# Kernel optimization log

Hardware: AMD Instinct MI355X
Metric: run time of the kernel (lower is better)

Reference implementation:

```python
import jax, jax.numpy as jnp
import numpy as np

D = 1024
N_HEADS = 16
HEAD = D // N_HEADS


def apply_rope(x):
    # x: [b, h, s, hd]
    b, h, s, hd = x.shape
    half = hd // 2
    pos = jnp.arange(1, s + 1, dtype=jnp.float32)  # positions start at 1 (as in source)
    thetas = 10000.0 ** (-2.0 * jnp.arange(half, dtype=jnp.float32) / hd)
    angles = pos[:, None] * thetas[None, :]  # [s, half]
    cos, sin = jnp.cos(angles), jnp.sin(angles)
    x_even, x_odd = x[..., 0::2], x[..., 1::2]
    out_even = x_even * cos - x_odd * sin
    out_odd = x_odd * cos + x_even * sin
    # interleave back: stack on new last axis then reshape
    return jnp.stack([out_even, out_odd], axis=-1).reshape(b, h, s, hd)


def setup_inputs() -> dict:
    key = jax.random.key(0)
    k1, k2, k3 = jax.random.split(key, 3)
    b, s = 4, 2048
    x = jax.random.normal(k1, (b, s, D), dtype=jnp.float32)
    # torch Linear(d, 3d, bias=False): y = x @ W.T; store as [d, 3d] so y = x @ W_qkv
    W_qkv = jax.random.normal(k2, (D, 3 * D), dtype=jnp.float32) * (1.0 / np.sqrt(D))
    W_out = jax.random.normal(k3, (D, D), dtype=jnp.float32) * (1.0 / np.sqrt(D))
    return {"x": x, "W_qkv": W_qkv, "W_out": W_out}


def reference(x, W_qkv, W_out):
    b, s, _ = x.shape
    qkv = x @ W_qkv  # [b, s, 3d]
    q, k, v = jnp.split(qkv, 3, axis=-1)

    def split_heads(t):
        return t.reshape(b, s, N_HEADS, HEAD).transpose(0, 2, 1, 3)  # [b,h,s,hd]

    q, k, v = split_heads(q), split_heads(k), split_heads(v)
    q, k = apply_rope(q), apply_rope(k)
    scale = 1.0 / np.sqrt(HEAD)
    scores = jnp.einsum("bhqd,bhkd->bhqk", q, k) * scale
    attn = jax.nn.softmax(scores, axis=-1)
    out = jnp.einsum("bhqk,bhkd->bhqd", attn, v)  # [b,h,s,hd]
    out = out.transpose(0, 2, 1, 3).reshape(b, s, D)
    return out @ W_out
```

## Files before the change

### kernel.cpp

```cpp
#include <hip/hip_runtime.h>
#include <hip/hip_bf16.h>
#include <math.h>

#define BB 4
#define SS 2048
#define DD 1024
#define NH 16
#define HD 64

typedef __attribute__((ext_vector_type(8))) short bf16x8;
typedef __attribute__((ext_vector_type(4))) float f32x4;

#define MFMA16(a, b, c) __builtin_amdgcn_mfma_f32_16x16x32_bf16(a, b, c, 0, 0, 0)

#if __has_builtin(__builtin_amdgcn_exp2f)
#define EXP2(x) __builtin_amdgcn_exp2f(x)
#else
#define EXP2(x) exp2f(x)
#endif

__device__ __forceinline__ ushort f2bf(float f) {
    unsigned int u = __builtin_bit_cast(unsigned int, f);
    u += 0x7FFF + ((u >> 16) & 1);
    return (ushort)(u >> 16);
}
__device__ __forceinline__ float bf2f(ushort u) {
    return __builtin_bit_cast(float, (unsigned)u << 16);
}
__device__ __forceinline__ unsigned pk2bf(float a, float b) {
    __hip_bfloat162 h = __float22bfloat162_rn(make_float2(a, b));
    unsigned r;
    __builtin_memcpy(&r, &h, 4);
    return r;
}

__device__ __forceinline__ void gload16(const void* g, void* l) {
    __builtin_amdgcn_global_load_lds(
        (const __attribute__((address_space(1))) void*)g,
        (__attribute__((address_space(3))) void*)l, 16, 0, 0);
}

__global__ __launch_bounds__(256)
void prep_kernel(const float* __restrict__ X, ushort* __restrict__ Xb,
                 const float* __restrict__ Wqkv, ushort* __restrict__ Wqt,
                 const float* __restrict__ Wout, ushort* __restrict__ Wot,
                 float2* __restrict__ tab)
{
    const int blk = blockIdx.x;
    const int t = threadIdx.x;
    if (blk < 4096) {
        const size_t i = ((size_t)blk * 256 + t) * 8;
        const float4 v0 = *(const float4*)&X[i];
        const float4 v1 = *(const float4*)&X[i + 4];
        uint4 o;
        o.x = pk2bf(v0.x, v0.y);
        o.y = pk2bf(v0.z, v0.w);
        o.z = pk2bf(v1.x, v1.y);
        o.w = pk2bf(v1.z, v1.w);
        *(uint4*)&Xb[i] = o;
    } else if (blk < 5120) {
        __shared__ ushort T[64][72];
        const bool isQ = blk < 4864;
        const int b2 = isQ ? blk - 4096 : blk - 4864;
        const int ncols = isQ ? 3072 : 1024;
        const float* W = isQ ? Wqkv : Wout;
        ushort* Wt = isQ ? Wqt : Wot;
        const int ki = b2 / (ncols / 64), ni = b2 % (ncols / 64);
        const int k0 = ki * 64, n0 = ni * 64;
        #pragma unroll
        for (int e = 0; e < 4; ++e) {
            const int idx = t + e * 256;
            const int kr = idx >> 4, c4 = (idx & 15) * 4;
            const float4 v = *(const float4*)&W[(size_t)(k0 + kr) * ncols + n0 + c4];
            T[c4 + 0][kr] = f2bf(v.x); T[c4 + 1][kr] = f2bf(v.y);
            T[c4 + 2][kr] = f2bf(v.z); T[c4 + 3][kr] = f2bf(v.w);
        }
        __syncthreads();
        #pragma unroll
        for (int e = 0; e < 2; ++e) {
            const int idx = t + e * 256;
            const int nr = idx >> 3, kc = (idx & 7) * 8;
            uint4 o;
            o.x = (unsigned)T[nr][kc + 0] | ((unsigned)T[nr][kc + 1] << 16);
            o.y = (unsigned)T[nr][kc + 2] | ((unsigned)T[nr][kc + 3] << 16);
            o.z = (unsigned)T[nr][kc + 4] | ((unsigned)T[nr][kc + 5] << 16);
            o.w = (unsigned)T[nr][kc + 6] | ((unsigned)T[nr][kc + 7] << 16);
            *(uint4*)&Wt[(size_t)(n0 + nr) * 1024 + k0 + kc] = o;
        }
    } else {
        const int id = (blk - 5120) * 256 + t;
        const int s = id >> 5, i = id & 31;
        const float theta = expf(-0.28782313662425572f * (float)i);
        const float ang = (float)(s + 1) * theta;
        float sn, cs;
        sincosf(ang, &sn, &cs);
        tab[id] = make_float2(cs, sn);
    }
}

__global__ __launch_bounds__(256)
void rope_cast_kernel(ushort* __restrict__ Qi, ushort* __restrict__ Ki,
                      const float2* __restrict__ tab)
{
    const int HALFT = BB * NH * SS * 8;
    const int tid = blockIdx.x * 256 + threadIdx.x;
    const bool isK = tid >= HALFT;
    const int rr = isK ? tid - HALFT : tid;
    ushort* buf = isK ? Ki : Qi;
    const float sc = isK ? 1.0f : 0.180336880111112f;

    const int row = rr >> 3;
    const int e8  = rr & 7;
    const int s   = row & (SS - 1);
    const size_t base = (size_t)row * HD + e8 * 8;
    const uint4 iv = *(const uint4*)&buf[base];
    const unsigned ua[4] = {iv.x, iv.y, iv.z, iv.w};

    uint4 o;
    unsigned ow[4];
    #pragma unroll
    for (int j = 0; j < 4; ++j) {
        const float xe = __builtin_bit_cast(float, ua[j] << 16);
        const float xo = __builtin_bit_cast(float, ua[j] & 0xffff0000u);
        const float2 cs = tab[s * 32 + e8 * 4 + j];
        const float oe = (xe * cs.x - xo * cs.y) * sc;
        const float oo = (xo * cs.x + xe * cs.y) * sc;
        ow[j] = pk2bf(oe, oo);
    }
    o.x = ow[0]; o.y = ow[1]; o.z = ow[2]; o.w = ow[3];
    *(uint4*)&buf[base] = o;
}

template<int K, int NI>
__global__ __launch_bounds__(256)
void gemm_bt_kernel(const ushort* __restrict__ Ag, const ushort* __restrict__ Btg,
                    ushort* __restrict__ D0, ushort* __restrict__ D1,
                    ushort* __restrict__ D2)
{
    __shared__ ushort Ab[2][128 * 32];
    __shared__ ushort Bb[2][128 * 32];
    const int t = threadIdx.x, lane = t & 63, w = t >> 6;
    const int lo = lane & 15, g = lane >> 4;
    const int wr = w >> 1, wc = w & 1;

    const int nwg = gridDim.x;
    const int bid = blockIdx.x;
    const int wg = (bid & 7) * (nwg >> 3) + (bid >> 3);
    const int m0 = (wg / NI) * 128, n0 = (wg % NI) * 128;

    const int srow  = lane >> 2;
    const int sslot = (lane & 3) ^ ((srow >> 1) & 3);

    f32x4 acc[4][4];
    #pragma unroll
    for (int m = 0; m < 4; ++m)
        #pragma unroll
        for (int n = 0; n < 4; ++n)
            acc[m][n] = (f32x4){0.f, 0.f, 0.f, 0.f};

#define STAGE(kt, bb)                                                              \
    {                                                                              \
        const int kk = (kt) * 32;                                                  \
        _Pragma("unroll")                                                          \
        for (int e = 0; e < 2; ++e) {                                              \
            const int r0 = w * 32 + e * 16;                                        \
            gload16(Ag  + (size_t)(m0 + r0 + srow) * K + kk + sslot * 8,           \
                    &Ab[bb][r0 * 32]);                                             \
            gload16(Btg + (size_t)(n0 + r0 + srow) * K + kk + sslot * 8,           \
                    &Bb[bb][r0 * 32]);                                             \
        }                                                                          \
    }

    const int NKS = K / 32;
    STAGE(0, 0)
    for (int kt = 0; kt < NKS; ++kt) {
        const int cur = kt & 1;
        if (kt + 1 < NKS) {
            STAGE(kt + 1, cur ^ 1)
            asm volatile("s_waitcnt vmcnt(4)" ::: "memory");
        } else {
            asm volatile("s_waitcnt vmcnt(0)" ::: "memory");
        }
        __builtin_amdgcn_sched_barrier(0);
        __builtin_amdgcn_s_barrier();

        const int xsl = ((g ^ ((lo >> 1) & 3)) << 3);
        bf16x8 af[4], bfr[4];
        #pragma unroll
        for (int m = 0; m < 4; ++m)
            af[m] = *(const bf16x8*)&Ab[cur][(wr * 64 + m * 16 + lo) * 32 + xsl];
        #pragma unroll
        for (int n = 0; n < 4; ++n)
            bfr[n] = *(const bf16x8*)&Bb[cur][(wc * 64 + n * 16 + lo) * 32 + xsl];
        #pragma unroll
        for (int m = 0; m < 4; ++m)
            #pragma unroll
            for (int n = 0; n < 4; ++n)
                acc[m][n] = MFMA16(af[m], bfr[n], acc[m][n]);

        asm volatile("s_waitcnt lgkmcnt(0)" ::: "memory");
        __builtin_amdgcn_sched_barrier(0);
        __builtin_amdgcn_s_barrier();
    }
#undef STAGE

    const int tensor = n0 >> 10;
    const int cb = n0 & 1023;
    if (tensor == 2) {
        #pragma unroll
        for (int m = 0; m < 4; ++m) {
            const int row0 = m0 + wr * 64 + m * 16 + g * 4;
            const int b = row0 >> 11, sbase = row0 & (SS - 1);
            #pragma unroll
            for (int n = 0; n < 4; ++n) {
                const int c = cb + wc * 64 + n * 16 + lo;
                const int h = c >> 6, d = c & 63;
                uint2 wv = make_uint2(pk2bf(acc[m][n][0], acc[m][n][1]),
                                      pk2bf(acc[m][n][2], acc[m][n][3]));
                *(uint2*)&D2[(((size_t)b * NH + h) * HD + d) * SS + sbase] = wv;
            }
        }
    } else {
        ushort* dst = (tensor == 0) ? D0 : D1;
        const bool evlane = (lo & 1) == 0;
        #pragma unroll
        for (int m = 0; m < 4; ++m)
            #pragma unroll
            for (int n = 0; n < 4; ++n) {
                const int c = cb + wc * 64 + n * 16 + lo;
                const int h = c >> 6, d = c & 63;
                #pragma unroll
                for (int r = 0; r < 4; ++r) {
                    const int row = m0 + wr * 64 + m * 16 + g * 4 + r;
                    const float x  = acc[m][n][r];
                    const float xp = __shfl_xor(x, 1);
                    if (evlane) {
                        const int b = row >> 11, s = row & (SS - 1);
                        *(unsigned*)&dst[(((size_t)b * NH + h) * SS + s) * HD + d] =
                            pk2bf(x, xp);
                    }
                }
            }
    }
}

template<int K>
__global__ __launch_bounds__(256)
void gemm_bt64_kernel(const ushort* __restrict__ Ag, const ushort* __restrict__ Btg,
                      float* __restrict__ Df)
{
    __shared__ ushort Ab[2][128 * 32];
    __shared__ ushort Bb[2][64 * 32];
    const int t = threadIdx.x, lane = t & 63, w = t >> 6;
    const int lo = lane & 15, g = lane >> 4;
    const int NI = 16;

    const int nwg = gridDim.x;
    const int bid = blockIdx.x;
    const int wg = (bid & 7) * (nwg >> 3) + (bid >> 3);
    const int m0 = (wg / NI) * 128, n0 = (wg % NI) * 64;

    const int srow  = lane >> 2;
    const int sslot = (lane & 3) ^ ((srow >> 1) & 3);

    f32x4 acc[2][4];
    #pragma unroll
    for (int m = 0; m < 2; ++m)
        #pragma unroll
        for (int n = 0; n < 4; ++n)
            acc[m][n] = (f32x4){0.f, 0.f, 0.f, 0.f};

#define STAGE(kt, bb)                                                              \
    {                                                                              \
        const int kk = (kt) * 32;                                                  \
        _Pragma("unroll")                                                          \
        for (int e = 0; e < 2; ++e) {                                              \
            const int r0 = w * 32 + e * 16;                                        \
            gload16(Ag + (size_t)(m0 + r0 + srow) * K + kk + sslot * 8,            \
                    &Ab[bb][r0 * 32]);                                             \
        }                                                                          \
        gload16(Btg + (size_t)(n0 + w * 16 + srow) * K + kk + sslot * 8,           \
                &Bb[bb][(w * 16) * 32]);                                           \
    }

    const int NKS = K / 32;
    STAGE(0, 0)
    for (int kt = 0; kt < NKS; ++kt) {
        const int cur = kt & 1;
        if (kt + 1 < NKS) {
            STAGE(kt + 1, cur ^ 1)
            asm volatile("s_waitcnt vmcnt(3)" ::: "memory");
        } else {
            asm volatile("s_waitcnt vmcnt(0)" ::: "memory");
        }
        __builtin_amdgcn_sched_barrier(0);
        __builtin_amdgcn_s_barrier();

        const int xsl = ((g ^ ((lo >> 1) & 3)) << 3);
        bf16x8 af[2], bfr[4];
        #pragma unroll
        for (int m = 0; m < 2; ++m)
            af[m] = *(const bf16x8*)&Ab[cur][(w * 32 + m * 16 + lo) * 32 + xsl];
        #pragma unroll
        for (int n = 0; n < 4; ++n)
            bfr[n] = *(const bf16x8*)&Bb[cur][(n * 16 + lo) * 32 + xsl];
        #pragma unroll
        for (int m = 0; m < 2; ++m)
            #pragma unroll
            for (int n = 0; n < 4; ++n)
                acc[m][n] = MFMA16(af[m], bfr[n], acc[m][n]);

        asm volatile("s_waitcnt lgkmcnt(0)" ::: "memory");
        __builtin_amdgcn_sched_barrier(0);
        __builtin_amdgcn_s_barrier();
    }
#undef STAGE

    const bool evlane = (lo & 1) == 0;
    #pragma unroll
    for (int m = 0; m < 2; ++m)
        #pragma unroll
        for (int n = 0; n < 4; ++n) {
            const int col = n0 + n * 16 + lo;
            #pragma unroll
            for (int r = 0; r < 4; ++r) {
                const int row = m0 + w * 32 + m * 16 + g * 4 + r;
                const float x  = acc[m][n][r];
                const float xp = __shfl_xor(x, 1);
                if (evlane)
                    *(float2*)&Df[(size_t)row * 1024 + col] = make_float2(x, xp);
            }
        }
}

__global__ __launch_bounds__(256, 4)
void attn_mfma_kernel(const ushort* __restrict__ Qbf, const ushort* __restrict__ Kbf,
                      const ushort* __restrict__ Vt, ushort* __restrict__ Obt)
{
    __shared__ ushort Ks[2][4096];
    __shared__ ushort Vs[2][4096];
    __shared__ ushort Ps[4][1024];

    const int t    = threadIdx.x;
    const int lane = t & 63;
    const int w    = t >> 6;
    const int g    = lane >> 4;
    const int lo   = lane & 15;
    const int lo7  = lo & 7;
    const int wmask = lo & 6;

    const int i  = blockIdx.x;
    const int r_ = i & 63;
    const int bh = (r_ & 7) * 8 + (r_ >> 3);
    const int qt = i >> 6;

    const size_t kbase  = (size_t)bh * SS * HD;
    const size_t vtbase = (size_t)bh * HD * SS;
    const int s0 = qt * 128;

    bf16x8 qa[2][2];
    #pragma unroll
    for (int qh = 0; qh < 2; ++qh)
        #pragma unroll
        for (int df = 0; df < 2; ++df)
            qa[qh][df] = *(const bf16x8*)
                &Qbf[kbase + (size_t)(s0 + w * 32 + qh * 16 + lo) * HD + df * 32 + g * 8];

    f32x4 Oc[2][4];
    #pragma unroll
    for (int qh = 0; qh < 2; ++qh)
        #pragma unroll
        for (int nb = 0; nb < 4; ++nb)
            Oc[qh][nb] = (f32x4){0.f, 0.f, 0.f, 0.f};
    f32x4 lacc[2];
    lacc[0] = (f32x4){0.f, 0.f, 0.f, 0.f};
    lacc[1] = (f32x4){0.f, 0.f, 0.f, 0.f};
    const bf16x8 ones = {16256, 16256, 16256, 16256, 16256, 16256, 16256, 16256};

    const int srcsw = ((lane & 7) ^ (lane >> 3)) * 8;
    const int rowin = (lane >> 3);

    #define STAGE(kt, bb)                                                          \
    {                                                                              \
        _Pragma("unroll")                                                          \
        for (int e = 0; e < 2; ++e) {                                              \
            const int rw = w * 16 + e * 8;                                         \
            gload16(&Kbf[kbase + (size_t)((kt) * 64 + rw + rowin) * HD + srcsw],   \
                    &Ks[bb][rw * 64]);                                             \
            gload16(&Vt[vtbase + (size_t)(rw + rowin) * SS + (kt) * 64 + srcsw],   \
                    &Vs[bb][rw * 64]);                                             \
        }                                                                          \
    }

    const int NT = SS / 64;
    STAGE(0, 0)

    for (int kt = 0; kt < NT; ++kt) {
        const int cur = kt & 1;
        if (kt + 1 < NT) {
            STAGE(kt + 1, cur ^ 1)
            asm volatile("s_waitcnt vmcnt(4)" ::: "memory");
        } else {
            asm volatile("s_waitcnt vmcnt(0)" ::: "memory");
        }
        __builtin_amdgcn_sched_barrier(0);
        __builtin_amdgcn_s_barrier();

        f32x4 St[2][4];
        __builtin_amdgcn_s_setprio(1);
        #pragma unroll
        for (int k16 = 0; k16 < 4; ++k16) {
            const int row = k16 * 16 + lo;
            const int cb = row * 64;
            const bf16x8 k0 = *(const bf16x8*)&Ks[cur][cb + (((0 + g) ^ lo7) * 8)];
            const bf16x8 k1 = *(const bf16x8*)&Ks[cur][cb + (((4 + g) ^ lo7) * 8)];
            const f32x4 z = {0.f, 0.f, 0.f, 0.f};
            St[0][k16] = MFMA16(k0, qa[0][0], z);
            St[0][k16] = MFMA16(k1, qa[0][1], St[0][k16]);
            St[1][k16] = MFMA16(k0, qa[1][0], z);
            St[1][k16] = MFMA16(k1, qa[1][1], St[1][k16]);
        }
        __builtin_amdgcn_s_setprio(0);

        #pragma unroll
        for (int qh = 0; qh < 2; ++qh)
            #pragma unroll
            for (int k16 = 0; k16 < 4; ++k16)
                #pragma unroll
                for (int r = 0; r < 4; ++r)
                    St[qh][k16][r] = EXP2(St[qh][k16][r]);

        #pragma unroll
        for (int h = 0; h < 2; ++h) {
            #pragma unroll
            for (int qh = 0; qh < 2; ++qh) {
                const int q32 = qh * 16 + lo;
                #pragma unroll
                for (int kr = 0; kr < 2; ++kr) {
                    const f32x4 s4 = St[qh][2 * h + kr];
                    const uint2 wv = make_uint2(pk2bf(s4[0], s4[1]),
                                                pk2bf(s4[2], s4[3]));
                    const int sw = (kr * 4 + g) ^ wmask;
                    *(uint2*)&Ps[w][q32 * 32 + sw * 4] = wv;
                }
            }
            bf16x8 vf[4];
            #pragma unroll
            for (int nb = 0; nb < 4; ++nb)
                vf[nb] = *(const bf16x8*)
                    &Vs[cur][(nb * 16 + lo) * 64 + (((h * 4 + g) ^ lo7) * 8)];
            __builtin_amdgcn_s_setprio(1);
            #pragma unroll
            for (int qh = 0; qh < 2; ++qh) {
                const bf16x8 pa = *(const bf16x8*)
                    &Ps[w][(qh * 16 + lo) * 32 + (((2 * g) ^ wmask) * 4)];
                lacc[qh] = MFMA16(pa, ones, lacc[qh]);
                #pragma unroll
                for (int nb = 0; nb < 4; ++nb)
                    Oc[qh][nb] = MFMA16(pa, vf[nb], Oc[qh][nb]);
            }
            __builtin_amdgcn_s_setprio(0);
        }

        asm volatile("s_waitcnt lgkmcnt(0)" ::: "memory");
        __builtin_amdgcn_sched_barrier(0);
        __builtin_amdgcn_s_barrier();
    }

    const int b = bh >> 4, h = bh & 15;
    #pragma unroll
    for (int qh = 0; qh < 2; ++qh) {
        #pragma unroll
        for (int r = 0; r < 4; ++r) {
            const float inv = 1.0f / lacc[qh][r];
            const int srow = s0 + w * 32 + qh * 16 + g * 4 + r;
            const size_t rbase = (size_t)(b * SS + srow) * 1024 + h * HD;
            #pragma unroll
            for (int nb = 0; nb < 4; ++nb)
                Obt[rbase + nb * 16 + lo] = f2bf(Oc[qh][nb][r] * inv);
        }
    }
    #undef STAGE
}

extern "C" void kernel_launch(void* const* d_in, const int* in_sizes, int n_in,
                              void* d_out, int out_size, void* d_ws, size_t ws_size,
                              hipStream_t stream)
{
    const float* x    = (const float*)d_in[0];
    const float* Wqkv = (const float*)d_in[1];
    const float* Wout = (const float*)d_in[2];
    float* out = (float*)d_out;

    const size_t TEN = (size_t)BB * NH * SS * HD;
    ushort* u = (ushort*)d_ws;
    ushort* Qb16 = u;
    ushort* Kb16 = u + TEN;
    ushort* Vt   = u + 2 * TEN;
    ushort* Obt  = u + 3 * TEN;
    ushort* Xb   = u + 4 * TEN;
    ushort* Wqt  = u + 5 * TEN;
    ushort* Wot  = u + 5 * TEN + 3145728;
    float2* tab  = (float2*)(u + 5 * TEN + 3145728 + 1048576);

    prep_kernel<<<dim3(4096 + 768 + 256 + 256), 256, 0, stream>>>(
        x, Xb, Wqkv, Wqt, Wout, Wot, tab);

    gemm_bt_kernel<1024, 24><<<dim3(64 * 24), 256, 0, stream>>>(
        Xb, Wqt, Qb16, Kb16, Vt);

    rope_cast_kernel<<<dim3(2 * BB * NH * SS * 8 / 256), 256, 0, stream>>>(
        Qb16, Kb16, tab);

    attn_mfma_kernel<<<dim3(BB * NH * (SS / 128)), 256, 0, stream>>>(
        Qb16, Kb16, Vt, Obt);

    gemm_bt64_kernel<1024><<<dim3(64 * 16), 256, 0, stream>>>(Obt, Wot, out);
}
```

Measured before the change: 209.6 us.

## Keep attention probabilities in registers by permuting V k-order instead of LDS round-trip

Removes the per-warp shared-memory staging buffer for the softmax probabilities. The S^T accumulator fragments are packed straight into the bf16 A operand for the PV MFMA, and the V fragment loads are split into two 8-byte LDS reads so their k ordering matches the register layout of P. This cuts LDS writes and reads plus the associated waits, and frees shared memory, at the cost of twice as many (narrower) V reads from LDS.

```diff
diff --git a/kernel.cpp b/kernel.cpp
--- a/kernel.cpp
+++ b/kernel.cpp
@@ -339,7 +339,6 @@
 {
     __shared__ ushort Ks[2][4096];
     __shared__ ushort Vs[2][4096];
-    __shared__ ushort Ps[4][1024];
 
     const int t    = threadIdx.x;
     const int lane = t & 63;
@@ -347,7 +346,6 @@
     const int g    = lane >> 4;
     const int lo   = lane & 15;
     const int lo7  = lo & 7;
-    const int wmask = lo & 6;
 
     const int i  = blockIdx.x;
     const int r_ = i & 63;
@@ -431,29 +429,28 @@
                     St[qh][k16][r] = EXP2(St[qh][k16][r]);
 
         #pragma unroll
-        for (int h = 0; h < 2; ++h) {
+        for (int ph = 0; ph < 2; ++ph) {
+            bf16x8 vf[4];
+            #pragma unroll
+            for (int nb = 0; nb < 4; ++nb) {
+                const int rb = (nb * 16 + lo) * 64 + (g & 1) * 4;
+                const uint2 vlo = *(const uint2*)
+                    &Vs[cur][rb + (((ph * 4 + (g >> 1)) ^ lo7) * 8)];
+                const uint2 vhi = *(const uint2*)
+                    &Vs[cur][rb + (((ph * 4 + (g >> 1) + 2) ^ lo7) * 8)];
+                const uint4 vv = make_uint4(vlo.x, vlo.y, vhi.x, vhi.y);
+                __builtin_memcpy(&vf[nb], &vv, 16);
+            }
+            __builtin_amdgcn_s_setprio(1);
             #pragma unroll
             for (int qh = 0; qh < 2; ++qh) {
-                const int q32 = qh * 16 + lo;
-                #pragma unroll
-                for (int kr = 0; kr < 2; ++kr) {
-                    const f32x4 s4 = St[qh][2 * h + kr];
-                    const uint2 wv = make_uint2(pk2bf(s4[0], s4[1]),
-                                                pk2bf(s4[2], s4[3]));
-                    const int sw = (kr * 4 + g) ^ wmask;
-                    *(uint2*)&Ps[w][q32 * 32 + sw * 4] = wv;
-                }
-            }
-            bf16x8 vf[4];
-            #pragma unroll
-            for (int nb = 0; nb < 4; ++nb)
-                vf[nb] = *(const bf16x8*)
-                    &Vs[cur][(nb * 16 + lo) * 64 + (((h * 4 + g) ^ lo7) * 8)];
-            __builtin_amdgcn_s_setprio(1);
-            #pragma unroll
-            for (int qh = 0; qh < 2; ++qh) {
-                const bf16x8 pa = *(const bf16x8*)
-                    &Ps[w][(qh * 16 + lo) * 32 + (((2 * g) ^ wmask) * 4)];
+                uint4 pu;
+                pu.x = pk2bf(St[qh][2 * ph][0], St[qh][2 * ph][1]);
+                pu.y = pk2bf(St[qh][2 * ph][2], St[qh][2 * ph][3]);
+                pu.z = pk2bf(St[qh][2 * ph + 1][0], St[qh][2 * ph + 1][1]);
+                pu.w = pk2bf(St[qh][2 * ph + 1][2], St[qh][2 * ph + 1][3]);
+                bf16x8 pa;
+                __builtin_memcpy(&pa, &pu, 16);
                 lacc[qh] = MFMA16(pa, ones, lacc[qh]);
                 #pragma unroll
                 for (int nb = 0; nb < 4; ++nb)
```

New measurement: 209.0 us. Within noise of the previous version (-0.3%).
